# Kernel tuning notes

Measured on AMD Instinct MI355X. Metric: run time of the kernel, lower is better.

## Reference

```python
import jax, jax.numpy as jnp
import numpy as np

B, D, K, H, W = 2, 512, 32, 64, 64


def setup_inputs() -> dict:
    key = jax.random.key(0)
    k1, k2, k3 = jax.random.split(key, 3)
    X = jax.random.normal(k1, (B, D, H, W), dtype=jnp.float32)
    std1 = 1.0 / (K * D) ** 0.5
    codewords = jax.random.uniform(k2, (K, D), minval=-std1, maxval=std1, dtype=jnp.float32)
    scale = jax.random.uniform(k3, (D, K), minval=-1.0, maxval=0.0, dtype=jnp.float32)
    return {"X": X, "codewords": codewords, "scale": scale}


def reference(X, codewords, scale):
    # X: [B, D, H, W] -> x: [B, N, D], N = H*W
    Bv, Dv = X.shape[0], X.shape[1]
    x = X.reshape(Bv, Dv, -1).transpose(0, 2, 1)            # [B, N, D]
    # broadcast residual: x[b,n,d] - codewords[k,d], scaled per (d,k)
    residual = (x[:, :, :, None] - codewords.T) * scale     # [B, N, D, K]
    # soft assignment over K codewords
    Q = jax.nn.softmax(-0.5 * jnp.sum(residual * residual, axis=2), axis=2)  # [B, N, K]
    # weighted aggregation over N, normalized by per-codeword mass
    Z_num = jnp.einsum('bnk,bndk->bdk', Q, residual)        # [B, D, K]
    Z_ = Z_num / Q.sum(axis=1)[:, None, :]                  # [B, D, K]
    # L2-normalize along D
    Z = Z_ / jnp.sqrt(jnp.sum(Z_ * Z_, axis=1, keepdims=True))
    return (Z, Q)
```

## Files before the change

### kernel.cpp

```cpp
#include <hip/hip_runtime.h>
#include <math.h>

#define B_DIM 2
#define D_DIM 512
#define K_DIM 32
#define N_DIM 4096

typedef float v2f __attribute__((ext_vector_type(2)));

__device__ __forceinline__ void pk_bl(v2f& d, v2f a, v2f b) {
    asm("v_pk_fma_f32 %0, %1, %2, %0 op_sel:[0,0,0] op_sel_hi:[1,0,1]"
        : "+v"(d) : "v"(a), "v"(b));
}
__device__ __forceinline__ void pk_bh(v2f& d, v2f a, v2f b) {
    asm("v_pk_fma_f32 %0, %1, %2, %0 op_sel:[0,1,0] op_sel_hi:[1,1,1]"
        : "+v"(d) : "v"(a), "v"(b));
}

__global__ __launch_bounds__(256, 2)
void k_dist_q(const float* __restrict__ X, const float* __restrict__ CW,
              const float* __restrict__ SC, float* __restrict__ Qout,
              float* __restrict__ nsq, int* __restrict__ cnt)
{
    __shared__ __align__(16) float xlds[16 * 516];
    __shared__ __align__(16) float red[16 * 16 * 36];

    const int tid = threadIdx.x;
    const int b  = blockIdx.x >> 8;
    const int n0 = (blockIdx.x & 255) << 4;
    const int dp = tid & 63;
    const int kp = tid >> 6;
    const int k0 = kp << 3;

    if (blockIdx.x == 0) {
        if (tid < 64) nsq[tid] = 0.f;
        if (tid == 64) *cnt = 0;
    }

    const float* xsrc = X + (size_t)b * D_DIM * N_DIM + n0;
#pragma unroll
    for (int j = 0; j < 8; ++j) {
        const int d  = (tid >> 2) + (j << 6);
        const int n4 = (tid & 3) << 2;
        float4 v = *(const float4*)(xsrc + (size_t)d * N_DIM + n4);
        xlds[(n4 + 0) * 516 + d] = v.x;
        xlds[(n4 + 1) * 516 + d] = v.y;
        xlds[(n4 + 2) * 516 + d] = v.z;
        xlds[(n4 + 3) * 516 + d] = v.w;
    }

    float cv[8][8];
#pragma unroll
    for (int kk = 0; kk < 8; ++kk) {
        const float* cr = CW + (k0 + kk) * D_DIM + (dp << 2);
        float4 c0 = *(const float4*)(cr);
        float4 c1 = *(const float4*)(cr + 256);
        cv[kk][0] = c0.x; cv[kk][1] = c0.y; cv[kk][2] = c0.z; cv[kk][3] = c0.w;
        cv[kk][4] = c1.x; cv[kk][5] = c1.y; cv[kk][6] = c1.z; cv[kk][7] = c1.w;
    }
    v2f A2[8][4], B2r[8][4], ckp2[4];
#pragma unroll
    for (int kk2 = 0; kk2 < 4; ++kk2) ckp2[kk2] = (v2f)(0.f);
#pragma unroll
    for (int dd = 0; dd < 8; ++dd) {
        const int d = (dd < 4) ? ((dp << 2) + dd) : (256 + (dp << 2) + (dd - 4));
        float4 s0 = *(const float4*)(SC + d * K_DIM + k0);
        float4 s1 = *(const float4*)(SC + d * K_DIM + k0 + 4);
        float sv[8] = {s0.x, s0.y, s0.z, s0.w, s1.x, s1.y, s1.z, s1.w};
#pragma unroll
        for (int kk2 = 0; kk2 < 4; ++kk2) {
#pragma unroll
            for (int h = 0; h < 2; ++h) {
                const int kk = 2 * kk2 + h;
                float c = cv[kk][dd];
                float a = sv[kk] * sv[kk];
                A2[dd][kk2][h]  = a;
                B2r[dd][kk2][h] = -2.f * a * c;
                ckp2[kk2][h] = fmaf(a * c, c, ckp2[kk2][h]);
            }
        }
    }
    __syncthreads();

#pragma unroll
    for (int n = 0; n < 16; ++n) {
        v2f d2[4];
#pragma unroll
        for (int kk2 = 0; kk2 < 4; ++kk2) d2[kk2] = ckp2[kk2];
        float4 xa = *(const float4*)(&xlds[n * 516 + (dp << 2)]);
        float4 xb = *(const float4*)(&xlds[n * 516 + (dp << 2) + 256]);
        v2f xp[4] = {{xa.x, xa.y}, {xa.z, xa.w}, {xb.x, xb.y}, {xb.z, xb.w}};
#pragma unroll
        for (int dq = 0; dq < 4; ++dq) {
            v2f x2p = xp[dq] * xp[dq];
#pragma unroll
            for (int kk2 = 0; kk2 < 4; ++kk2) {
                pk_bl(d2[kk2], A2[2 * dq][kk2],      x2p);
                pk_bl(d2[kk2], B2r[2 * dq][kk2],     xp[dq]);
                pk_bh(d2[kk2], A2[2 * dq + 1][kk2],  x2p);
                pk_bh(d2[kk2], B2r[2 * dq + 1][kk2], xp[dq]);
            }
        }
        float dist[8] = {d2[0].x, d2[0].y, d2[1].x, d2[1].y,
                         d2[2].x, d2[2].y, d2[3].x, d2[3].y};
#pragma unroll
        for (int kk = 0; kk < 8; ++kk) {
            dist[kk] += __shfl_xor(dist[kk], 32);
            dist[kk] += __shfl_xor(dist[kk], 16);
        }
        if (dp < 16) {
            float* r = &red[(n * 16 + dp) * 36 + k0];
            *(float4*)(r)     = make_float4(dist[0], dist[1], dist[2], dist[3]);
            *(float4*)(r + 4) = make_float4(dist[4], dist[5], dist[6], dist[7]);
        }
    }
    __syncthreads();

#pragma unroll
    for (int h = 0; h < 2; ++h) {
        const int n = (tid >> 5) + (h << 3);
        const int k = tid & 31;
        float dsum = 0.f;
#pragma unroll
        for (int i = 0; i < 16; ++i) dsum += red[(n * 16 + i) * 36 + k];
        float m = dsum;
#pragma unroll
        for (int mk = 16; mk >= 1; mk >>= 1)
            m = fminf(m, __shfl_xor(m, mk));
        float e = __expf(-0.5f * (dsum - m));
        float ssum = e;
#pragma unroll
        for (int mk = 16; mk >= 1; mk >>= 1)
            ssum += __shfl_xor(ssum, mk);
        Qout[((size_t)b * N_DIM + n0 + n) * K_DIM + k] = __fdividef(e, ssum);
    }
}

__global__ __launch_bounds__(256, 2)
void k_tpart(const float* __restrict__ X, const float* __restrict__ Qin,
             float* __restrict__ TP, float* __restrict__ Mpart)
{
    __shared__ __align__(16) float Xs[64 * 68];
    __shared__ __align__(16) float Qs[64 * 36];
    __shared__ __align__(16) float red4[4 * 64 * 36];
    __shared__ float mred[8][33];

    const int tid = threadIdx.x;
    const int bid = blockIdx.x;
    const int ns = bid & 31;
    const int dt = (bid >> 5) & 7;
    const int b  = bid >> 8;
    const int nsub = tid >> 5;
    const int dp = tid & 7;
    const int kp = (tid >> 3) & 3;
    const int k0t = kp << 3;
    const int wv = tid >> 6;

    v2f acc2[8][4];
#pragma unroll
    for (int i = 0; i < 8; ++i)
#pragma unroll
        for (int j = 0; j < 4; ++j) acc2[i][j] = (v2f)(0.f);

    const float* xsrc = X + ((size_t)b * D_DIM + dt * 64) * N_DIM + ns * 128;
    const float* qsrc = Qin + ((size_t)b * N_DIM + ns * 128) * K_DIM;

    for (int ch = 0; ch < 2; ++ch) {
        __syncthreads();
#pragma unroll
        for (int i = 0; i < 4; ++i) {
            int flat4 = tid + (i << 8);
            int row = flat4 >> 4;
            int c4  = (flat4 & 15) << 2;
            float4 v = *(const float4*)(xsrc + (size_t)row * N_DIM + (ch << 6) + c4);
            *(float4*)(&Xs[row * 68 + c4]) = v;
        }
#pragma unroll
        for (int i = 0; i < 2; ++i) {
            int flat4 = tid + (i << 8);
            int nn = flat4 >> 3;
            int k4 = (flat4 & 7) << 2;
            *(float4*)(&Qs[nn * 36 + k4]) =
                *(const float4*)(qsrc + ((ch << 6) + nn) * K_DIM + k4);
        }
        __syncthreads();
#pragma unroll
        for (int s = 0; s < 2; ++s) {
            const int nb = (nsub << 3) + (s << 2);
            float4 xr[8];
#pragma unroll
            for (int i = 0; i < 8; ++i)
                xr[i] = *(const float4*)(&Xs[(dp + (i << 3)) * 68 + nb]);
#pragma unroll
            for (int n = 0; n < 4; ++n) {
                float4 qa = *(const float4*)(&Qs[(nb + n) * 36 + k0t]);
                float4 qb = *(const float4*)(&Qs[(nb + n) * 36 + k0t + 4]);
                v2f q2[4] = {{qa.x, qa.y}, {qa.z, qa.w}, {qb.x, qb.y}, {qb.z, qb.w}};
#pragma unroll
                for (int i = 0; i < 8; ++i) {
                    v2f xlo = {xr[i].x, xr[i].y};
                    v2f xhi = {xr[i].z, xr[i].w};
                    v2f xb2 = (n < 2) ? xlo : xhi;
                    if ((n & 1) == 0) {
#pragma unroll
                        for (int j = 0; j < 4; ++j) pk_bl(acc2[i][j], q2[j], xb2);
                    } else {
#pragma unroll
                        for (int j = 0; j < 4; ++j) pk_bh(acc2[i][j], q2[j], xb2);
                    }
                }
            }
        }
    }
    __syncthreads();
#pragma unroll
    for (int i = 0; i < 8; ++i)
#pragma unroll
        for (int j = 0; j < 4; ++j) {
            acc2[i][j].x += __shfl_xor(acc2[i][j].x, 32);
            acc2[i][j].y += __shfl_xor(acc2[i][j].y, 32);
        }
    if ((tid & 32) == 0) {
#pragma unroll
        for (int i = 0; i < 8; ++i) {
            float* r = &red4[(wv * 64 + dp + (i << 3)) * 36 + k0t];
            *(float4*)(r)     = make_float4(acc2[i][0].x, acc2[i][0].y,
                                            acc2[i][1].x, acc2[i][1].y);
            *(float4*)(r + 4) = make_float4(acc2[i][2].x, acc2[i][2].y,
                                            acc2[i][3].x, acc2[i][3].y);
        }
    }
    __syncthreads();
    float* dst = TP + (((size_t)ns * 2 + b) * D_DIM + dt * 64) * K_DIM;
#pragma unroll
    for (int e = 0; e < 8; ++e) {
        int flat = tid + (e << 8);
        int dl = flat >> 5;
        int k  = flat & 31;
        float s = red4[(0 * 64 + dl) * 36 + k] + red4[(1 * 64 + dl) * 36 + k]
                + red4[(2 * 64 + dl) * 36 + k] + red4[(3 * 64 + dl) * 36 + k];
        dst[dl * K_DIM + k] = s;
    }
    if (dt == 0) {
        const int k = tid & 31, g = tid >> 5;
        float qm = 0.f;
#pragma unroll
        for (int n = 0; n < 16; ++n)
            qm += qsrc[(g * 16 + n) * K_DIM + k];
        mred[g][k] = qm;
        __syncthreads();
        if (tid < K_DIM) {
            float t = 0.f;
#pragma unroll
            for (int i = 0; i < 8; ++i) t += mred[i][tid];
            Mpart[(ns * B_DIM + b) * K_DIM + tid] = t;
        }
    }
}

__global__ __launch_bounds__(256)
void k_zfuse(const float* __restrict__ TP, const float* __restrict__ Mpart,
             const float* __restrict__ CW, const float* __restrict__ SC,
             float* __restrict__ Z, float* __restrict__ nsq, int* __restrict__ cnt)
{
    __shared__ float part[8][33];
    const int tid = threadIdx.x;
    const int b  = blockIdx.x >> 6;
    const int ds = blockIdx.x & 63;
    const int d  = (ds << 3) + (tid >> 5);
    const int k  = tid & 31;
    float sum = 0.f;
#pragma unroll
    for (int ns = 0; ns < 32; ++ns)
        sum += TP[(((size_t)ns * 2 + b) * D_DIM + d) * K_DIM + k];
    float m = 0.f;
#pragma unroll
    for (int ns = 0; ns < 32; ++ns)
        m += Mpart[(ns * B_DIM + b) * K_DIM + k];
    float c = CW[k * D_DIM + d];
    float s = SC[d * K_DIM + k];
    float z = s * (sum / m - c);
    part[tid >> 5][k] = z * z;
    __syncthreads();
    if (tid < K_DIM) {
        float t = 0.f;
#pragma unroll
        for (int i = 0; i < 8; ++i) t += part[i][tid];
        atomicAdd(&nsq[b * K_DIM + tid], t);
    }
    __syncthreads();
    if (tid == 0) {
        __hip_atomic_fetch_add(cnt, 1, __ATOMIC_ACQ_REL, __HIP_MEMORY_SCOPE_AGENT);
        while (__hip_atomic_load(cnt, __ATOMIC_ACQUIRE, __HIP_MEMORY_SCOPE_AGENT) < 128)
            __builtin_amdgcn_s_sleep(1);
    }
    __syncthreads();
    float nv = __hip_atomic_load(&nsq[b * K_DIM + k], __ATOMIC_RELAXED,
                                 __HIP_MEMORY_SCOPE_AGENT);
    Z[((b * D_DIM) + d) * K_DIM + k] = z * rsqrtf(nv);
}

extern "C" void kernel_launch(void* const* d_in, const int* in_sizes, int n_in,
                              void* d_out, int out_size, void* d_ws, size_t ws_size,
                              hipStream_t stream)
{
    const float* X  = (const float*)d_in[0];
    const float* CW = (const float*)d_in[1];
    const float* SC = (const float*)d_in[2];
    float* Z = (float*)d_out;
    float* Q = (float*)d_out + B_DIM * D_DIM * K_DIM;

    float* W    = (float*)d_ws;
    float* nsq  = W;
    int*   cnt  = (int*)(W + 64);
    float* Mpart= W + 128;
    float* TP   = W + 128 + 2048;

    k_dist_q<<<512, 256, 0, stream>>>(X, CW, SC, Q, nsq, cnt);
    k_tpart <<<512, 256, 0, stream>>>(X, Q, TP, Mpart);
    k_zfuse <<<128, 256, 0, stream>>>(TP, Mpart, CW, SC, Z, nsq, cnt);
}
```

Measured before the change: 99.31 us.

## Precompute scale/codeword tables in prep kernel and retile distance computation

Adds a small prep kernel that computes the A=s^2, B=-2s^2c and per-codeword constant tables once, instead of every distance block rebuilding them from CW and SC. The distance kernel is retiled so each thread holds a 4n x 4k register tile over a 64-wide D slice. It reads A/B from global/L2 and X from LDS stored d-major without the transpose, then reduces 8 partial sums in LDS. This trades per-block setup and shuffle reductions for an extra kernel launch and more global reads of the tables.

```diff
diff --git a/kernel.cpp b/kernel.cpp
--- a/kernel.cpp
+++ b/kernel.cpp
@@ -17,112 +17,111 @@
         : "+v"(d) : "v"(a), "v"(b));
 }
 
+__global__ __launch_bounds__(256)
+void k_prep(const float* __restrict__ CW, const float* __restrict__ SC,
+            float* __restrict__ A, float* __restrict__ B2,
+            float* __restrict__ CK, float* __restrict__ zeroes)
+{
+    __shared__ float ckred[8][33];
+    const int tid = threadIdx.x;
+    const int idx = blockIdx.x * 256 + tid;
+    const int d = idx >> 5, k = idx & 31;
+    float s = SC[idx];
+    float c = CW[k * D_DIM + d];
+    float a = s * s;
+    A[idx]  = a;
+    B2[idx] = -2.f * a * c;
+    if (blockIdx.x == 0) {
+        if (tid < 128) zeroes[tid] = 0.f;
+        const int kk = tid & 31, g = tid >> 5;
+        float acc = 0.f;
+        for (int dd = g * 64; dd < g * 64 + 64; ++dd) {
+            float sv = SC[dd * K_DIM + kk];
+            float cv = CW[kk * D_DIM + dd];
+            acc = fmaf(sv * sv * cv, cv, acc);
+        }
+        ckred[g][kk] = acc;
+        __syncthreads();
+        if (tid < 32) {
+            float t = 0.f;
+#pragma unroll
+            for (int i = 0; i < 8; ++i) t += ckred[i][tid];
+            CK[tid] = t;
+        }
+    }
+}
+
 __global__ __launch_bounds__(256, 2)
-void k_dist_q(const float* __restrict__ X, const float* __restrict__ CW,
-              const float* __restrict__ SC, float* __restrict__ Qout,
-              float* __restrict__ nsq, int* __restrict__ cnt)
-{
-    __shared__ __align__(16) float xlds[16 * 516];
-    __shared__ __align__(16) float red[16 * 16 * 36];
+void k_dist_q(const float* __restrict__ X, const float* __restrict__ At,
+              const float* __restrict__ Bt, const float* __restrict__ CK,
+              float* __restrict__ Qout)
+{
+    __shared__ __align__(16) float xlds[D_DIM * 16];
+    __shared__ __align__(16) float part[8 * 16 * 36];
 
     const int tid = threadIdx.x;
     const int b  = blockIdx.x >> 8;
     const int n0 = (blockIdx.x & 255) << 4;
-    const int dp = tid & 63;
-    const int kp = tid >> 6;
-    const int k0 = kp << 3;
-
-    if (blockIdx.x == 0) {
-        if (tid < 64) nsq[tid] = 0.f;
-        if (tid == 64) *cnt = 0;
-    }
 
     const float* xsrc = X + (size_t)b * D_DIM * N_DIM + n0;
 #pragma unroll
     for (int j = 0; j < 8; ++j) {
         const int d  = (tid >> 2) + (j << 6);
         const int n4 = (tid & 3) << 2;
-        float4 v = *(const float4*)(xsrc + (size_t)d * N_DIM + n4);
-        xlds[(n4 + 0) * 516 + d] = v.x;
-        xlds[(n4 + 1) * 516 + d] = v.y;
-        xlds[(n4 + 2) * 516 + d] = v.z;
-        xlds[(n4 + 3) * 516 + d] = v.w;
-    }
-
-    float cv[8][8];
-#pragma unroll
-    for (int kk = 0; kk < 8; ++kk) {
-        const float* cr = CW + (k0 + kk) * D_DIM + (dp << 2);
-        float4 c0 = *(const float4*)(cr);
-        float4 c1 = *(const float4*)(cr + 256);
-        cv[kk][0] = c0.x; cv[kk][1] = c0.y; cv[kk][2] = c0.z; cv[kk][3] = c0.w;
-        cv[kk][4] = c1.x; cv[kk][5] = c1.y; cv[kk][6] = c1.z; cv[kk][7] = c1.w;
-    }
-    v2f A2[8][4], B2r[8][4], ckp2[4];
-#pragma unroll
-    for (int kk2 = 0; kk2 < 4; ++kk2) ckp2[kk2] = (v2f)(0.f);
-#pragma unroll
-    for (int dd = 0; dd < 8; ++dd) {
-        const int d = (dd < 4) ? ((dp << 2) + dd) : (256 + (dp << 2) + (dd - 4));
-        float4 s0 = *(const float4*)(SC + d * K_DIM + k0);
-        float4 s1 = *(const float4*)(SC + d * K_DIM + k0 + 4);
-        float sv[8] = {s0.x, s0.y, s0.z, s0.w, s1.x, s1.y, s1.z, s1.w};
-#pragma unroll
-        for (int kk2 = 0; kk2 < 4; ++kk2) {
-#pragma unroll
-            for (int h = 0; h < 2; ++h) {
-                const int kk = 2 * kk2 + h;
-                float c = cv[kk][dd];
-                float a = sv[kk] * sv[kk];
-                A2[dd][kk2][h]  = a;
-                B2r[dd][kk2][h] = -2.f * a * c;
-                ckp2[kk2][h] = fmaf(a * c, c, ckp2[kk2][h]);
+        *(float4*)(&xlds[d * 16 + n4]) =
+            *(const float4*)(xsrc + (size_t)d * N_DIM + n4);
+    }
+
+    const int ks  = tid & 7;
+    const int ng  = (tid >> 3) & 3;
+    const int dsl = tid >> 5;
+
+    float acc[4][4];
+#pragma unroll
+    for (int n = 0; n < 4; ++n)
+#pragma unroll
+        for (int k = 0; k < 4; ++k) acc[n][k] = 0.f;
+
+    const float* arow = At + ((dsl << 6) * K_DIM) + (ks << 2);
+    const float* brow = Bt + ((dsl << 6) * K_DIM) + (ks << 2);
+    __syncthreads();
+    const float* xrow = &xlds[(dsl << 6) * 16 + (ng << 2)];
+
+    for (int i = 0; i < 64; i += 8) {
+#pragma unroll
+        for (int u = 0; u < 8; ++u) {
+            const int d = i + u;
+            float4 a4 = *(const float4*)(arow + d * K_DIM);
+            float4 b4 = *(const float4*)(brow + d * K_DIM);
+            float4 x4 = *(const float4*)(xrow + d * 16);
+            float av[4] = {a4.x, a4.y, a4.z, a4.w};
+            float bv[4] = {b4.x, b4.y, b4.z, b4.w};
+            float xv[4] = {x4.x, x4.y, x4.z, x4.w};
+#pragma unroll
+            for (int n = 0; n < 4; ++n) {
+                const float x  = xv[n];
+                const float x2 = x * x;
+#pragma unroll
+                for (int k = 0; k < 4; ++k)
+                    acc[n][k] = fmaf(av[k], x2, fmaf(bv[k], x, acc[n][k]));
             }
         }
     }
-    __syncthreads();
-
-#pragma unroll
-    for (int n = 0; n < 16; ++n) {
-        v2f d2[4];
-#pragma unroll
-        for (int kk2 = 0; kk2 < 4; ++kk2) d2[kk2] = ckp2[kk2];
-        float4 xa = *(const float4*)(&xlds[n * 516 + (dp << 2)]);
-        float4 xb = *(const float4*)(&xlds[n * 516 + (dp << 2) + 256]);
-        v2f xp[4] = {{xa.x, xa.y}, {xa.z, xa.w}, {xb.x, xb.y}, {xb.z, xb.w}};
-#pragma unroll
-        for (int dq = 0; dq < 4; ++dq) {
-            v2f x2p = xp[dq] * xp[dq];
-#pragma unroll
-            for (int kk2 = 0; kk2 < 4; ++kk2) {
-                pk_bl(d2[kk2], A2[2 * dq][kk2],      x2p);
-                pk_bl(d2[kk2], B2r[2 * dq][kk2],     xp[dq]);
-                pk_bh(d2[kk2], A2[2 * dq + 1][kk2],  x2p);
-                pk_bh(d2[kk2], B2r[2 * dq + 1][kk2], xp[dq]);
-            }
-        }
-        float dist[8] = {d2[0].x, d2[0].y, d2[1].x, d2[1].y,
-                         d2[2].x, d2[2].y, d2[3].x, d2[3].y};
-#pragma unroll
-        for (int kk = 0; kk < 8; ++kk) {
-            dist[kk] += __shfl_xor(dist[kk], 32);
-            dist[kk] += __shfl_xor(dist[kk], 16);
-        }
-        if (dp < 16) {
-            float* r = &red[(n * 16 + dp) * 36 + k0];
-            *(float4*)(r)     = make_float4(dist[0], dist[1], dist[2], dist[3]);
-            *(float4*)(r + 4) = make_float4(dist[4], dist[5], dist[6], dist[7]);
-        }
-    }
+
+    __syncthreads();
+#pragma unroll
+    for (int nj = 0; nj < 4; ++nj)
+        *(float4*)(&part[(dsl * 16 + (ng << 2) + nj) * 36 + (ks << 2)]) =
+            make_float4(acc[nj][0], acc[nj][1], acc[nj][2], acc[nj][3]);
     __syncthreads();
 
 #pragma unroll
     for (int h = 0; h < 2; ++h) {
         const int n = (tid >> 5) + (h << 3);
         const int k = tid & 31;
-        float dsum = 0.f;
-#pragma unroll
-        for (int i = 0; i < 16; ++i) dsum += red[(n * 16 + i) * 36 + k];
+        float dsum = CK[k];
+#pragma unroll
+        for (int i = 0; i < 8; ++i) dsum += part[(i * 16 + n) * 36 + k];
         float m = dsum;
 #pragma unroll
         for (int mk = 16; mk >= 1; mk >>= 1)
@@ -315,8 +314,12 @@
     int*   cnt  = (int*)(W + 64);
     float* Mpart= W + 128;
     float* TP   = W + 128 + 2048;
-
-    k_dist_q<<<512, 256, 0, stream>>>(X, CW, SC, Q, nsq, cnt);
+    float* At   = TP + 32 * B_DIM * D_DIM * K_DIM;
+    float* Bt   = At + D_DIM * K_DIM;
+    float* CKt  = Bt + D_DIM * K_DIM;
+
+    k_prep  <<< 64, 256, 0, stream>>>(CW, SC, At, Bt, CKt, W);
+    k_dist_q<<<512, 256, 0, stream>>>(X, At, Bt, CKt, Q);
     k_tpart <<<512, 256, 0, stream>>>(X, Q, TP, Mpart);
     k_zfuse <<<128, 256, 0, stream>>>(TP, Mpart, CW, SC, Z, nsq, cnt);
 }
```

Measured after the change: 102.8 us. +3.5%, slower.
